# Optimization experiments

Hardware: AMD Instinct MI355X
Metric: run time of the kernel (lower is better)

## Reference

```python
import jax, jax.numpy as jnp
import numpy as np

B = 4096          # batch_size * world_size
D = 256           # embedding dim
TEMP = 0.5        # temperature
EPS = 1e-8        # torch CosineSimilarity eps


def setup_inputs() -> dict:
    key = jax.random.key(0)
    k1, k2 = jax.random.split(key)
    z_i = jax.random.normal(k1, (B, D), dtype=jnp.float32)
    z_j = jax.random.normal(k2, (B, D), dtype=jnp.float32)
    return {"z_i": z_i, "z_j": z_j}


def reference(z_i, z_j):
    N = 2 * B
    z = jnp.concatenate([z_i, z_j], axis=0)                      # [N, D]
    # Cosine similarity: normalize rows (clamped norm like torch eps), then matmul.
    norms = jnp.maximum(jnp.linalg.norm(z, axis=1, keepdims=True), EPS)
    zn = z / norms
    sim = jnp.matmul(zn, zn.T) / TEMP                            # [N, N]
    # Positive pairs: offsets +B and -B from the diagonal.
    pos = jnp.concatenate([jnp.diagonal(sim, B), jnp.diagonal(sim, -B)])  # [N]
    # Cross-entropy with label 0 over [pos, negatives]:
    # logsumexp over {pos} U {negatives} == logsumexp over row excluding the diagonal
    # (the (i, i±B) entries removed by the mask are exactly re-added as the positive).
    neg_inf = jnp.array(-jnp.inf, dtype=sim.dtype)
    sim_nodiag = jnp.where(jnp.eye(N, dtype=bool), neg_inf, sim)
    lse = jax.nn.logsumexp(sim_nodiag, axis=1)                   # [N]
    loss = jnp.sum(lse - pos) / N                                # reduction='sum' then /N
    return loss
```

## Files before the change

### kernel.cpp

```cpp
#include <hip/hip_runtime.h>

#define NROWS 8192
#define DIM   256
#define BHALF 4096
#define NCHUNK 8
#define SCALE 1.69864358f
#define LN2F  0.69314718f

typedef unsigned char u8;
typedef __attribute__((ext_vector_type(16))) float f32x16;
typedef __attribute__((ext_vector_type(4))) int   i32x4;
typedef __attribute__((ext_vector_type(8))) int   i32x8;

__device__ inline void gload_lds16(const void* g, void* l) {
  __builtin_amdgcn_global_load_lds(
      (const __attribute__((address_space(1))) void*)g,
      (__attribute__((address_space(3))) void*)l, 16, 0, 0);
}

__device__ inline float fp8_to_f32(int b) {
  const int e = (b >> 3) & 15, m = b & 7;
  float mag = e ? __builtin_bit_cast(float, ((e + 120) << 23) | (m << 20))
                : (float)m * 0x1p-9f;
  return (b & 128) ? -mag : mag;
}

__global__ __launch_bounds__(256) void nrm_kernel(const float* __restrict__ zi,
                                                  const float* __restrict__ zj,
                                                  u8* __restrict__ zn8,
                                                  float* __restrict__ rowsum,
                                                  float* __restrict__ pos,
                                                  float* __restrict__ diag,
                                                  int* __restrict__ cnt,
                                                  float* __restrict__ out) {
  const int t = threadIdx.x, b = blockIdx.x;
  const int gid = b * 256 + t;
  if (gid < NROWS) rowsum[gid] = 0.f;
  if (gid < 64) cnt[gid] = 0;
  if (gid == 0) out[0] = 0.f;

  const int w = t >> 6, l = t & 63;
#pragma unroll
  for (int q = 0; q < 2; ++q) {
    const int p = b * 8 + w * 2 + q;
    float4 vi = *(const float4*)(zi + (size_t)p * DIM + l * 4);
    float4 vj = *(const float4*)(zj + (size_t)p * DIM + l * 4);
    float ssi = vi.x * vi.x + vi.y * vi.y + vi.z * vi.z + vi.w * vi.w;
    float ssj = vj.x * vj.x + vj.y * vj.y + vj.z * vj.z + vj.w * vj.w;
#pragma unroll
    for (int m = 1; m < 64; m <<= 1) {
      ssi += __shfl_xor(ssi, m);
      ssj += __shfl_xor(ssj, m);
    }
    const float invi = SCALE / fmaxf(sqrtf(ssi), 1e-8f);
    const float invj = SCALE / fmaxf(sqrtf(ssj), 1e-8f);
    int pi = __builtin_amdgcn_cvt_pk_fp8_f32(vi.x * invi, vi.y * invi, 0, false);
    pi = __builtin_amdgcn_cvt_pk_fp8_f32(vi.z * invi, vi.w * invi, pi, true);
    int pj = __builtin_amdgcn_cvt_pk_fp8_f32(vj.x * invj, vj.y * invj, 0, false);
    pj = __builtin_amdgcn_cvt_pk_fp8_f32(vj.z * invj, vj.w * invj, pj, true);
    *(int*)(zn8 + (size_t)p * DIM + l * 4) = pi;
    *(int*)(zn8 + (size_t)(p + BHALF) * DIM + l * 4) = pj;

    float dot = 0.f, di = 0.f, dj = 0.f;
#pragma unroll
    for (int k2 = 0; k2 < 4; ++k2) {
      const float qi = fp8_to_f32((pi >> (8 * k2)) & 255);
      const float qj = fp8_to_f32((pj >> (8 * k2)) & 255);
      dot += qi * qj; di += qi * qi; dj += qj * qj;
    }
#pragma unroll
    for (int m = 1; m < 64; m <<= 1) {
      dot += __shfl_xor(dot, m);
      di  += __shfl_xor(di, m);
      dj  += __shfl_xor(dj, m);
    }
    if      (l == 0) pos[p] = dot * LN2F;
    else if (l == 1) pos[p + BHALF] = dot * LN2F;
    else if (l == 2) diag[p] = di;
    else if (l == 3) diag[p + BHALF] = dj;
  }
}

__global__ __launch_bounds__(256, 2) void sim_kernel(const u8* __restrict__ zn8,
                                                     float* __restrict__ rowsum,
                                                     const float* __restrict__ pos,
                                                     const float* __restrict__ diag,
                                                     int* __restrict__ cnt,
                                                     float* __restrict__ out) {
  __shared__ __align__(16) u8 Bsm[2][128 * DIM];
  __shared__ float plane[4][128];
  __shared__ float wsum[2];
  __shared__ int sfin;

  const int t = threadIdx.x;
  const int w = t >> 6, l = t & 63;
  const int n31 = l & 31, kh = l >> 5;

  const int rp = (int)blockIdx.x >> 3;
  const int ch = (int)blockIdx.x & 7;
  const int colbase = ch * 1024;

  int soff[8], doff[8];
#pragma unroll
  for (int i = 0; i < 8; ++i) {
    int c = i * 256 + t;
    int r = c >> 4, cd = c & 15;
    int cs = (cd & 8) | ((cd ^ r) & 7);
    soff[i] = r * DIM + cs * 16;
    doff[i] = (i * 256 + w * 64) * 16;
  }
  auto STAGE = [&](int base_row, u8* dst) {
#pragma unroll
    for (int i = 0; i < 8; ++i)
      gload_lds16(zn8 + (size_t)base_row * DIM + soff[i], dst + doff[i]);
  };
  auto RD32 = [&](const u8* buf, int row, int kk) -> i32x8 {
    const int salt = row & 7;
    const u8* base = buf + row * DIM;
    const int c0 = kk * 4 + kh * 2;
    i32x4 lo = *(const i32x4*)(base + (((c0 & 8) | ((c0 ^ salt) & 7)) << 4));
    i32x4 hi = *(const i32x4*)(base + ((((c0 + 1) & 8) | (((c0 + 1) ^ salt) & 7)) << 4));
    return __builtin_shufflevector(lo, hi, 0, 1, 2, 3, 4, 5, 6, 7);
  };

  STAGE(rp * 128, &Bsm[0][0]);
  STAGE(colbase, &Bsm[1][0]);
  asm volatile("s_waitcnt vmcnt(8)" ::: "memory");
  __builtin_amdgcn_sched_barrier(0);
  __builtin_amdgcn_s_barrier();
  __builtin_amdgcn_sched_barrier(0);

  i32x8 pb[4][4];
#pragma unroll
  for (int pj = 0; pj < 4; ++pj)
#pragma unroll
    for (int kk = 0; kk < 4; ++kk)
      pb[pj][kk] = RD32(&Bsm[0][0], pj * 32 + n31, kk);
  asm volatile("s_waitcnt lgkmcnt(0)" ::: "memory");
  __builtin_amdgcn_sched_barrier(0);

  float rsum[4] = {0.f, 0.f, 0.f, 0.f};

#pragma unroll 2
  for (int ti = 0; ti < 8; ++ti) {
    asm volatile("s_waitcnt vmcnt(0)" ::: "memory");
    __builtin_amdgcn_sched_barrier(0);
    __builtin_amdgcn_s_barrier();
    __builtin_amdgcn_sched_barrier(0);

    const u8* Bb = &Bsm[(ti + 1) & 1][0];
    if (ti < 7) STAGE(colbase + (ti + 1) * 128, &Bsm[ti & 1][0]);

    f32x16 acc[4];
#pragma unroll
    for (int pj = 0; pj < 4; ++pj) acc[pj] = (f32x16)(0.f);

    i32x8 af0 = RD32(Bb, w * 32 + n31, 0);
    i32x8 af1;
#pragma unroll
    for (int kk = 0; kk < 4; ++kk) {
      if (kk < 3) {
        i32x8 nxt = RD32(Bb, w * 32 + n31, kk + 1);
        if (kk & 1) af0 = nxt; else af1 = nxt;
        asm volatile("s_waitcnt lgkmcnt(2)" ::: "memory");
      } else {
        asm volatile("s_waitcnt lgkmcnt(0)" ::: "memory");
      }
      __builtin_amdgcn_sched_barrier(0);
      const i32x8 a = (kk & 1) ? af1 : af0;
      __builtin_amdgcn_s_setprio(1);
#pragma unroll
      for (int pj = 0; pj < 4; ++pj)
        acc[pj] = __builtin_amdgcn_mfma_scale_f32_32x32x64_f8f6f4(
            a, pb[pj][kk], acc[pj],
            0, 0,
            0, 0x7f7f7f7f,
            0, 0x7f7f7f7f);
      __builtin_amdgcn_s_setprio(0);
    }

#pragma unroll
    for (int pj = 0; pj < 4; ++pj) {
      float e0 = 0.f, e1 = 0.f, e2 = 0.f, e3 = 0.f;
#pragma unroll
      for (int r16 = 0; r16 < 16; r16 += 4) {
        e0 += __builtin_amdgcn_exp2f(acc[pj][r16]);
        e1 += __builtin_amdgcn_exp2f(acc[pj][r16 + 1]);
        e2 += __builtin_amdgcn_exp2f(acc[pj][r16 + 2]);
        e3 += __builtin_amdgcn_exp2f(acc[pj][r16 + 3]);
      }
      rsum[pj] += (e0 + e1) + (e2 + e3);
    }
  }

#pragma unroll
  for (int pj = 0; pj < 4; ++pj) {
    rsum[pj] += __shfl_xor(rsum[pj], 32);
    if (l < 32) plane[w][pj * 32 + l] = rsum[pj];
  }
  __syncthreads();

  if (t < 128)
    atomicAdd(&rowsum[rp * 128 + t],
              (plane[0][t] + plane[1][t]) + (plane[2][t] + plane[3][t]));
  asm volatile("s_waitcnt vmcnt(0)" ::: "memory");
  __syncthreads();
  if (t == 0) sfin = (atomicAdd(&cnt[rp], 1) == NCHUNK - 1);
  __syncthreads();
  if (sfin) {
    float v = 0.f;
    if (t < 128) {
      const int r = rp * 128 + t;
      float s = atomicAdd(&rowsum[r], 0.f);
      v = logf(s - __builtin_amdgcn_exp2f(diag[r])) - pos[r];
    }
#pragma unroll
    for (int m = 1; m < 64; m <<= 1) v += __shfl_xor(v, m);
    if (l == 0 && t < 128) wsum[w] = v;
    __syncthreads();
    if (t == 0) atomicAdd(out, (wsum[0] + wsum[1]) * (1.f / NROWS));
  }
}

extern "C" void kernel_launch(void* const* d_in, const int* in_sizes, int n_in,
                              void* d_out, int out_size, void* d_ws, size_t ws_size,
                              hipStream_t stream) {
  const float* zi = (const float*)d_in[0];
  const float* zj = (const float*)d_in[1];

  u8*    zn8    = (u8*)d_ws;
  float* rowsum = (float*)((char*)d_ws + (size_t)NROWS * DIM);
  float* pos    = (float*)((char*)rowsum + (size_t)NROWS * 4);
  float* diag   = (float*)((char*)pos + (size_t)NROWS * 4);
  int*   cnt    = (int*)((char*)diag + (size_t)NROWS * 4);
  float* out    = (float*)d_out;

  nrm_kernel<<<512, 256, 0, stream>>>(zi, zj, zn8, rowsum, pos, diag, cnt, out);
  sim_kernel<<<64 * NCHUNK, 256, 0, stream>>>(zn8, rowsum, pos, diag, cnt, out);
}
```

Measured before the change: 31.71 us.

## Split sim tile work across eight waves with halved per-wave column tiles

The sim kernel moves from 256 to 512 threads per block. Each wave now computes a 32x64 output sub-tile (two MFMA accumulators) instead of 32x128, and staging drops to four LDS loads per thread. The A-fragment double-buffer prefetch is replaced by a simple load then wait before each MFMA group. The goal is more waves per CU to hide latency and less register pressure, at the cost of fewer MFMAs per wave between LDS waits and duplicated A-fragment reads across waves.

New measurement: 44.44 us. 40.1% more time.

```diff
diff --git a/kernel.cpp b/kernel.cpp
--- a/kernel.cpp
+++ b/kernel.cpp
@@ -81,7 +81,7 @@
   }
 }
 
-__global__ __launch_bounds__(256, 2) void sim_kernel(const u8* __restrict__ zn8,
+__global__ __launch_bounds__(512, 4) void sim_kernel(const u8* __restrict__ zn8,
                                                      float* __restrict__ rowsum,
                                                      const float* __restrict__ pos,
                                                      const float* __restrict__ diag,
@@ -94,25 +94,22 @@
 
   const int t = threadIdx.x;
   const int w = t >> 6, l = t & 63;
+  const int ws = w >> 1, wp = w & 1;
   const int n31 = l & 31, kh = l >> 5;
 
   const int rp = (int)blockIdx.x >> 3;
   const int ch = (int)blockIdx.x & 7;
   const int colbase = ch * 1024;
 
-  int soff[8], doff[8];
-#pragma unroll
-  for (int i = 0; i < 8; ++i) {
-    int c = i * 256 + t;
-    int r = c >> 4, cd = c & 15;
-    int cs = (cd & 8) | ((cd ^ r) & 7);
-    soff[i] = r * DIM + cs * 16;
-    doff[i] = (i * 256 + w * 64) * 16;
-  }
+  const int cd = t & 15;
+  const int cs = (cd & 8) | ((cd ^ (t >> 4)) & 7);
+  const int sbase = (t >> 4) * DIM + cs * 16;
+  const int dbase = t * 16;
   auto STAGE = [&](int base_row, u8* dst) {
 #pragma unroll
-    for (int i = 0; i < 8; ++i)
-      gload_lds16(zn8 + (size_t)base_row * DIM + soff[i], dst + doff[i]);
+    for (int i = 0; i < 4; ++i)
+      gload_lds16(zn8 + (size_t)base_row * DIM + sbase + i * 8192,
+                  dst + dbase + i * 8192);
   };
   auto RD32 = [&](const u8* buf, int row, int kk) -> i32x8 {
     const int salt = row & 7;
@@ -125,21 +122,22 @@
 
   STAGE(rp * 128, &Bsm[0][0]);
   STAGE(colbase, &Bsm[1][0]);
-  asm volatile("s_waitcnt vmcnt(8)" ::: "memory");
+  asm volatile("s_waitcnt vmcnt(4)" ::: "memory");
   __builtin_amdgcn_sched_barrier(0);
   __builtin_amdgcn_s_barrier();
   __builtin_amdgcn_sched_barrier(0);
 
-  i32x8 pb[4][4];
-#pragma unroll
-  for (int pj = 0; pj < 4; ++pj)
+  i32x8 pb[2][4];
+#pragma unroll
+  for (int pj = 0; pj < 2; ++pj)
 #pragma unroll
     for (int kk = 0; kk < 4; ++kk)
-      pb[pj][kk] = RD32(&Bsm[0][0], pj * 32 + n31, kk);
+      pb[pj][kk] = RD32(&Bsm[0][0], wp * 64 + pj * 32 + n31, kk);
   asm volatile("s_waitcnt lgkmcnt(0)" ::: "memory");
   __builtin_amdgcn_sched_barrier(0);
 
-  float rsum[4] = {0.f, 0.f, 0.f, 0.f};
+  float rsum[2] = {0.f, 0.f};
+  f32x16 z16 = (f32x16)(0.f);
 
 #pragma unroll 2
   for (int ti = 0; ti < 8; ++ti) {
@@ -151,28 +149,17 @@
     const u8* Bb = &Bsm[(ti + 1) & 1][0];
     if (ti < 7) STAGE(colbase + (ti + 1) * 128, &Bsm[ti & 1][0]);
 
-    f32x16 acc[4];
-#pragma unroll
-    for (int pj = 0; pj < 4; ++pj) acc[pj] = (f32x16)(0.f);
-
-    i32x8 af0 = RD32(Bb, w * 32 + n31, 0);
-    i32x8 af1;
+    f32x16 acc[2];
 #pragma unroll
     for (int kk = 0; kk < 4; ++kk) {
-      if (kk < 3) {
-        i32x8 nxt = RD32(Bb, w * 32 + n31, kk + 1);
-        if (kk & 1) af0 = nxt; else af1 = nxt;
-        asm volatile("s_waitcnt lgkmcnt(2)" ::: "memory");
-      } else {
-        asm volatile("s_waitcnt lgkmcnt(0)" ::: "memory");
-      }
+      i32x8 a = RD32(Bb, ws * 32 + n31, kk);
+      asm volatile("s_waitcnt lgkmcnt(0)" ::: "memory");
       __builtin_amdgcn_sched_barrier(0);
-      const i32x8 a = (kk & 1) ? af1 : af0;
       __builtin_amdgcn_s_setprio(1);
 #pragma unroll
-      for (int pj = 0; pj < 4; ++pj)
+      for (int pj = 0; pj < 2; ++pj)
         acc[pj] = __builtin_amdgcn_mfma_scale_f32_32x32x64_f8f6f4(
-            a, pb[pj][kk], acc[pj],
+            a, pb[pj][kk], (kk == 0) ? z16 : acc[pj],
             0, 0,
             0, 0x7f7f7f7f,
             0, 0x7f7f7f7f);
@@ -180,7 +167,7 @@
     }
 
 #pragma unroll
-    for (int pj = 0; pj < 4; ++pj) {
+    for (int pj = 0; pj < 2; ++pj) {
       float e0 = 0.f, e1 = 0.f, e2 = 0.f, e3 = 0.f;
 #pragma unroll
       for (int r16 = 0; r16 < 16; r16 += 4) {
@@ -194,9 +181,9 @@
   }
 
 #pragma unroll
-  for (int pj = 0; pj < 4; ++pj) {
+  for (int pj = 0; pj < 2; ++pj) {
     rsum[pj] += __shfl_xor(rsum[pj], 32);
-    if (l < 32) plane[w][pj * 32 + l] = rsum[pj];
+    if (l < 32) plane[ws][wp * 64 + pj * 32 + l] = rsum[pj];
   }
   __syncthreads();
 
@@ -236,5 +223,5 @@
   float* out    = (float*)d_out;
 
   nrm_kernel<<<512, 256, 0, stream>>>(zi, zj, zn8, rowsum, pos, diag, cnt, out);
-  sim_kernel<<<64 * NCHUNK, 256, 0, stream>>>(zn8, rowsum, pos, diag, cnt, out);
-}
+  sim_kernel<<<64 * NCHUNK, 512, 0, stream>>>(zn8, rowsum, pos, diag, cnt, out);
+}
```

## Give each wave private LDS column slices and drop block barriers in main loop

Applied to the files above, without the earlier changes.

Each wave now stages and reads only its own 32-row slice of the column tile in a per-wave LDS region, so the per-iteration block-wide s_barrier is removed and only vmcnt waits remain. The fixed row operand (pb) is loaded straight from global memory into registers instead of through LDS, and prefetch becomes two tiles ahead, issued after the MFMAs. The accumulator zeroing is folded into the first MFMA. The aim is less cross-wave synchronisation stall. The trade-off is that waves get no LDS data sharing, and correctness relies on global_load_lds writes being visible to the issuing wave's own LDS reads after only a vmcnt wait.

After: 71.43 us. 125% more time.

```diff
diff --git a/kernel.cpp b/kernel.cpp
--- a/kernel.cpp
+++ b/kernel.cpp
@@ -87,7 +87,7 @@
                                                      const float* __restrict__ diag,
                                                      int* __restrict__ cnt,
                                                      float* __restrict__ out) {
-  __shared__ __align__(16) u8 Bsm[2][128 * DIM];
+  __shared__ __align__(16) u8 Bsm[2][4][32 * DIM];
   __shared__ float plane[4][128];
   __shared__ float wsum[2];
   __shared__ int sfin;
@@ -100,67 +100,58 @@
   const int ch = (int)blockIdx.x & 7;
   const int colbase = ch * 1024;
 
-  int soff[8], doff[8];
-#pragma unroll
-  for (int i = 0; i < 8; ++i) {
-    int c = i * 256 + t;
-    int r = c >> 4, cd = c & 15;
-    int cs = (cd & 8) | ((cd ^ r) & 7);
-    soff[i] = r * DIM + cs * 16;
-    doff[i] = (i * 256 + w * 64) * 16;
-  }
-  auto STAGE = [&](int base_row, u8* dst) {
-#pragma unroll
-    for (int i = 0; i < 8; ++i)
-      gload_lds16(zn8 + (size_t)base_row * DIM + soff[i], dst + doff[i]);
+  auto STAGE = [&](int base_row, int d) {
+    u8* dst = &Bsm[d][w][0];
+#pragma unroll
+    for (int i = 0; i < 8; ++i) {
+      const int c = i * 64 + l;
+      const int r = c >> 4, cd = c & 15;
+      const int cs = (cd & 8) | ((cd ^ r) & 7);
+      gload_lds16(zn8 + (size_t)(base_row + r) * DIM + cs * 16,
+                  dst + i * 1024);
+    }
   };
-  auto RD32 = [&](const u8* buf, int row, int kk) -> i32x8 {
+  auto RD32 = [&](int d, int row, int kk) -> i32x8 {
     const int salt = row & 7;
-    const u8* base = buf + row * DIM;
+    const u8* base = &Bsm[d][w][0] + row * DIM;
     const int c0 = kk * 4 + kh * 2;
     i32x4 lo = *(const i32x4*)(base + (((c0 & 8) | ((c0 ^ salt) & 7)) << 4));
     i32x4 hi = *(const i32x4*)(base + ((((c0 + 1) & 8) | (((c0 + 1) ^ salt) & 7)) << 4));
     return __builtin_shufflevector(lo, hi, 0, 1, 2, 3, 4, 5, 6, 7);
   };
 
-  STAGE(rp * 128, &Bsm[0][0]);
-  STAGE(colbase, &Bsm[1][0]);
-  asm volatile("s_waitcnt vmcnt(8)" ::: "memory");
-  __builtin_amdgcn_sched_barrier(0);
-  __builtin_amdgcn_s_barrier();
-  __builtin_amdgcn_sched_barrier(0);
+  STAGE(colbase + w * 32, 0);
+  STAGE(colbase + 128 + w * 32, 1);
 
   i32x8 pb[4][4];
 #pragma unroll
   for (int pj = 0; pj < 4; ++pj)
 #pragma unroll
-    for (int kk = 0; kk < 4; ++kk)
-      pb[pj][kk] = RD32(&Bsm[0][0], pj * 32 + n31, kk);
-  asm volatile("s_waitcnt lgkmcnt(0)" ::: "memory");
-  __builtin_amdgcn_sched_barrier(0);
+    for (int kk = 0; kk < 4; ++kk) {
+      const u8* base = zn8 + (size_t)(rp * 128 + pj * 32 + n31) * DIM
+                       + kk * 64 + kh * 32;
+      i32x4 lo = *(const i32x4*)(base);
+      i32x4 hi = *(const i32x4*)(base + 16);
+      pb[pj][kk] = __builtin_shufflevector(lo, hi, 0, 1, 2, 3, 4, 5, 6, 7);
+    }
 
   float rsum[4] = {0.f, 0.f, 0.f, 0.f};
+  f32x16 z16 = (f32x16)(0.f);
 
 #pragma unroll 2
   for (int ti = 0; ti < 8; ++ti) {
-    asm volatile("s_waitcnt vmcnt(0)" ::: "memory");
+    if (ti < 7) asm volatile("s_waitcnt vmcnt(8)" ::: "memory");
+    else        asm volatile("s_waitcnt vmcnt(0)" ::: "memory");
     __builtin_amdgcn_sched_barrier(0);
-    __builtin_amdgcn_s_barrier();
-    __builtin_amdgcn_sched_barrier(0);
-
-    const u8* Bb = &Bsm[(ti + 1) & 1][0];
-    if (ti < 7) STAGE(colbase + (ti + 1) * 128, &Bsm[ti & 1][0]);
-
+
+    const int d = ti & 1;
     f32x16 acc[4];
-#pragma unroll
-    for (int pj = 0; pj < 4; ++pj) acc[pj] = (f32x16)(0.f);
-
-    i32x8 af0 = RD32(Bb, w * 32 + n31, 0);
+    i32x8 af0 = RD32(d, n31, 0);
     i32x8 af1;
 #pragma unroll
     for (int kk = 0; kk < 4; ++kk) {
       if (kk < 3) {
-        i32x8 nxt = RD32(Bb, w * 32 + n31, kk + 1);
+        i32x8 nxt = RD32(d, n31, kk + 1);
         if (kk & 1) af0 = nxt; else af1 = nxt;
         asm volatile("s_waitcnt lgkmcnt(2)" ::: "memory");
       } else {
@@ -172,12 +163,14 @@
 #pragma unroll
       for (int pj = 0; pj < 4; ++pj)
         acc[pj] = __builtin_amdgcn_mfma_scale_f32_32x32x64_f8f6f4(
-            a, pb[pj][kk], acc[pj],
+            a, pb[pj][kk], (kk == 0) ? z16 : acc[pj],
             0, 0,
             0, 0x7f7f7f7f,
             0, 0x7f7f7f7f);
       __builtin_amdgcn_s_setprio(0);
     }
+
+    if (ti < 6) STAGE(colbase + (ti + 2) * 128 + w * 32, d);
 
 #pragma unroll
     for (int pj = 0; pj < 4; ++pj) {
```
